# Performance work log

Measured on AMD Instinct MI355X. Metric: run time of the kernel, lower is better.

Reference implementation:

```python
import jax, jax.numpy as jnp
import numpy as np
import math

B, L, D, H = 4, 2048, 1024, 16
HD = D // H


def setup_inputs() -> dict:
    key = jax.random.key(0)
    k1, k2, k3 = jax.random.split(key, 3)
    x = jax.random.normal(k1, (B, L, D), dtype=jnp.float32)
    # Linear weights stored as [in, out] so y = x @ W (equivalent to torch x @ W.T)
    Wqkv = jax.random.normal(k2, (D, 3 * D), dtype=jnp.float32) * (1.0 / math.sqrt(D))
    Wproj = jax.random.normal(k3, (D, D), dtype=jnp.float32) * (1.0 / math.sqrt(D))
    attn_mask = jnp.tril(jnp.ones((L, L), dtype=bool))  # True = attend (causal)
    key_padding_mask = jnp.zeros((B, L), dtype=bool)     # True = padded (none here)
    return {"x": x, "Wqkv": Wqkv, "Wproj": Wproj,
            "attn_mask": attn_mask, "key_padding_mask": key_padding_mask}


def reference(x, Wqkv, Wproj, attn_mask, key_padding_mask):
    Bx, Lx, Dx = x.shape
    qkv = x @ Wqkv                              # [B, L, 3D]
    q, k, v = jnp.split(qkv, 3, axis=-1)
    def shape(t):
        return t.reshape(Bx, Lx, H, HD).transpose(0, 2, 1, 3)  # [B, H, L, hd]
    q, k, v = shape(q), shape(k), shape(v)
    att = jnp.einsum('bhqd,bhkd->bhqk', q, k) / math.sqrt(HD)  # [B, H, L, L]
    neg_inf = jnp.float32(-jnp.inf)
    att = jnp.where(attn_mask[None, None, :, :], att, neg_inf)
    att = jnp.where(key_padding_mask[:, None, None, :], neg_inf, att)
    att = jax.nn.softmax(att, axis=-1)
    y = jnp.einsum('bhqk,bhkd->bhqd', att, v)   # [B, H, L, hd]
    y = y.transpose(0, 2, 1, 3).reshape(Bx, Lx, Dx)
    return y @ Wproj
```

## Files before the change

### kernel.cpp

```cpp
#include <hip/hip_runtime.h>
#include <cstdint>
#include <cstddef>


typedef __attribute__((ext_vector_type(8))) __bf16 bf16x8;
typedef __attribute__((ext_vector_type(4))) __bf16 bf16x4;
typedef __attribute__((ext_vector_type(4))) float f32x4;
typedef __attribute__((ext_vector_type(16))) float f32x16;

__device__ __forceinline__ f32x4 mfma_bf16(bf16x8 a, bf16x8 b, f32x4 c) {
  return __builtin_amdgcn_mfma_f32_16x16x32_bf16(a, b, c, 0, 0, 0);
}

__device__ __forceinline__ f32x16 mfma32(bf16x8 a, bf16x8 b, f32x16 c) {
  return __builtin_amdgcn_mfma_f32_32x32x16_bf16(a, b, c, 0, 0, 0);
}

__device__ __forceinline__ unsigned cvtpk(float a, float b) {
  unsigned r;
  asm("v_cvt_pk_bf16_f32 %0, %1, %2" : "=v"(r) : "v"(a), "v"(b));
  return r;
}

__device__ __forceinline__ void async_copy16(const void* gsrc, void* ldsdst) {
  __builtin_amdgcn_global_load_lds(
      (const __attribute__((address_space(1))) void*)gsrc,
      (__attribute__((address_space(3))) void*)ldsdst, 16, 0, 0);
}

__global__ __launch_bounds__(256) void prep(
    const float* __restrict__ x, __bf16* __restrict__ xb,
    const float* __restrict__ Wqkv, __bf16* __restrict__ WqkvT,
    const float* __restrict__ Wproj, __bf16* __restrict__ WprojT) {
  const int bid = blockIdx.x;
  if (bid < 8192) {
    const size_t i = ((size_t)bid * 256 + threadIdx.x) * 4;
    const float4 v = *(const float4*)&x[i];
    bf16x4 o = {(__bf16)v.x, (__bf16)v.y, (__bf16)v.z, (__bf16)v.w};
    *(bf16x4*)&xb[i] = o;
    return;
  }
  __shared__ float tile[32][33];
  const float* in;
  __bf16* out;
  int idx, gx, R, C;
  if (bid < 8192 + 3072) {
    idx = bid - 8192; in = Wqkv; out = WqkvT; R = 1024; C = 3072; gx = 96;
  } else {
    idx = bid - 11264; in = Wproj; out = WprojT; R = 1024; C = 1024; gx = 32;
  }
  const int c0 = (idx % gx) * 32;
  const int r0 = (idx / gx) * 32;
  const int tx = threadIdx.x & 31;
  const int ty = threadIdx.x >> 5;
#pragma unroll
  for (int i = 0; i < 32; i += 8)
    tile[ty + i][tx] = in[(size_t)(r0 + ty + i) * C + c0 + tx];
  __syncthreads();
#pragma unroll
  for (int i = 0; i < 32; i += 8)
    out[(size_t)(c0 + ty + i) * R + r0 + tx] = (__bf16)tile[tx][ty + i];
}

#define GEMM128x128_CORE(Aptr, Bptr)                                         \
  const int srow32 = tid >> 3;                                    \
  const int schunk = ((tid & 7) ^ (srow32 & 7)) << 3;                        \
  const __bf16* aBase = &(Aptr)[(size_t)(m0 + srow32) * 1024 + schunk];      \
  const __bf16* bBase = &(Bptr)[(size_t)(n0 + srow32) * 1024 + schunk];      \
  auto stgTile = [&](int kt, int b2) {                                       \
    __bf16* dst = smem + b2 * 16384 + wave * 512;                            \
    _Pragma("unroll") for (int u = 0; u < 4; ++u)                            \
        async_copy16(aBase + (size_t)u * 32768 + kt * 64, dst + u * 2048);   \
    _Pragma("unroll") for (int u = 0; u < 4; ++u)                            \
        async_copy16(bBase + (size_t)u * 32768 + kt * 64,                    \
                     dst + 8192 + u * 2048);                                 \
  };                                                                         \
  const f32x4 zero = {0.f, 0.f, 0.f, 0.f};                                   \
  f32x4 acc[4][4];                                                           \
  _Pragma("unroll") for (int i = 0; i < 4; ++i)                              \
      _Pragma("unroll") for (int j = 0; j < 4; ++j) acc[i][j] = zero;        \
  stgTile(0, 0);                                                             \
  asm volatile("s_waitcnt vmcnt(0)" ::: "memory");                           \
  __builtin_amdgcn_s_barrier();                                              \
  for (int t = 0; t < 16; ++t) {                                             \
    const __bf16* As = smem + (t & 1) * 16384;                               \
    const __bf16* Bs = As + 8192;                                            \
    bf16x8 af[4][2], bfr[4][2];                                              \
    _Pragma("unroll") for (int mt = 0; mt < 4; ++mt)                         \
        _Pragma("unroll") for (int kk = 0; kk < 2; ++kk) af[mt][kk] =        \
            *(const bf16x8*)&As[(wr * 64 + mt * 16 + n16) * 64 +             \
                                (((kk * 4 + quad) ^ (n16 & 7)) << 3)];       \
    _Pragma("unroll") for (int nt = 0; nt < 4; ++nt)                         \
        _Pragma("unroll") for (int kk = 0; kk < 2; ++kk) bfr[nt][kk] =       \
            *(const bf16x8*)&Bs[(wc * 64 + nt * 16 + n16) * 64 +             \
                                (((kk * 4 + quad) ^ (n16 & 7)) << 3)];       \
    if (t < 15) stgTile(t + 1, (t + 1) & 1);                                 \
    __builtin_amdgcn_s_barrier();                                            \
    asm volatile("s_waitcnt lgkmcnt(0)" ::: "memory");                       \
    __builtin_amdgcn_sched_barrier(0);                                       \
    __builtin_amdgcn_s_setprio(1);                                           \
    _Pragma("unroll") for (int mt = 0; mt < 4; ++mt)                         \
        _Pragma("unroll") for (int nt = 0; nt < 4; ++nt)                     \
            _Pragma("unroll") for (int kk = 0; kk < 2; ++kk)                 \
                acc[mt][nt] = mfma_bf16(af[mt][kk], bfr[nt][kk],             \
                                        acc[mt][nt]);                        \
    __builtin_amdgcn_s_setprio(0);                                           \
    asm volatile("s_waitcnt vmcnt(0)" ::: "memory");                         \
    __builtin_amdgcn_s_barrier();                                            \
  }

__global__ __launch_bounds__(256, 2) void gemm_qkv(
    const __bf16* __restrict__ A, const __bf16* __restrict__ BT,
    __bf16* __restrict__ Q, __bf16* __restrict__ Kh, __bf16* __restrict__ VT) {
  extern __shared__ __bf16 smem[];
  const int wg = (blockIdx.x & 7) * 192 + (blockIdx.x >> 3);
  const int bm = wg / 24;
  const int bn = wg % 24;
  const int m0 = bm << 7;
  const int n0 = bn << 7;
  const int tid = threadIdx.x;
  const int wave = tid >> 6;
  const int lane = tid & 63;
  const int n16 = lane & 15;
  const int quad = lane >> 4;
  const int wr = wave >> 1;
  const int wc = wave & 1;

  GEMM128x128_CORE(A, BT)

  __bf16* tw = smem + wave * 2048;
  const int b = m0 >> 11;
  const int l0w = (m0 & 2047) + wr * 64;
  const int n = n0 + wc * 64;

  if (n < 2048) {
    const float QSCALE = 0.125f * 1.44269504089f;
    const bool isQ = (n < 1024);
    const int h = (n & 1023) >> 6;
    __bf16* dst = isQ ? Q : Kh;
    const size_t base = ((size_t)(b * 16 + h) * 2048) * 64;
#pragma unroll
    for (int pass = 0; pass < 2; ++pass) {
#pragma unroll
      for (int mt = 2 * pass; mt < 2 * pass + 2; ++mt) {
#pragma unroll
        for (int nt = 0; nt < 4; ++nt)
#pragma unroll
          for (int r = 0; r < 4; ++r) {
            const int hd = nt * 16 + n16;
            const int mm = (mt & 1) * 16 + quad * 4 + r;
            const float v = isQ ? acc[mt][nt][r] * QSCALE : acc[mt][nt][r];
            tw[mm * 64 + (((hd >> 3) ^ (mm & 7)) << 3) + (hd & 7)] =
                (__bf16)v;
          }
      }
#pragma unroll
      for (int i = 0; i < 4; ++i) {
        const int c = lane + 64 * i;
        const int row = c >> 3;
        const int hd0 = (c & 7) << 3;
        const int phys = (c & 7) ^ (row & 7);
        const bf16x8 v = *(const bf16x8*)&tw[row * 64 + phys * 8];
        *(bf16x8*)&dst[base + (size_t)(l0w + pass * 32 + row) * 64 + hd0] = v;
      }
    }
  } else {
    const int h = (n - 2048) >> 6;
    const size_t bhead = (size_t)(b * 16 + h);
#pragma unroll
    for (int pass = 0; pass < 2; ++pass) {
#pragma unroll
      for (int nt = 2 * pass; nt < 2 * pass + 2; ++nt) {
#pragma unroll
        for (int mt = 0; mt < 4; ++mt)
#pragma unroll
          for (int r = 0; r < 4; ++r) {
            const int hdp = (nt & 1) * 16 + n16;
            const int mm = mt * 16 + quad * 4 + r;
            const int phys = (mm >> 3) ^ (hdp & 7);
            tw[hdp * 64 + phys * 8 + (mm & 7)] = (__bf16)acc[mt][nt][r];
          }
      }
#pragma unroll
      for (int i = 0; i < 4; ++i) {
        const int c = lane + 64 * i;
        const int row = c >> 3;
        const int phys = (c & 7) ^ (row & 7);
        const bf16x8 v = *(const bf16x8*)&tw[row * 64 + phys * 8];
        *(bf16x8*)&VT[(bhead * 64 + pass * 32 + row) * 2048 + l0w +
                      (c & 7) * 8] = v;
      }
    }
  }
}

__global__ __launch_bounds__(256, 2) void gemm_bt_f32out(
    const __bf16* __restrict__ A, const __bf16* __restrict__ BT,
    float* __restrict__ C) {
  extern __shared__ __bf16 smem[];
  const int wg = (blockIdx.x & 7) * 64 + (blockIdx.x >> 3);
  const int bm = wg >> 3;
  const int bn = wg & 7;
  const int m0 = bm << 7;
  const int n0 = bn << 7;
  const int tid = threadIdx.x;
  const int wave = tid >> 6;
  const int lane = tid & 63;
  const int n16 = lane & 15;
  const int quad = lane >> 4;
  const int wr = wave >> 1;
  const int wc = wave & 1;

  GEMM128x128_CORE(A, BT)

#pragma unroll
  for (int mt = 0; mt < 4; ++mt) {
#pragma unroll
    for (int r = 0; r < 4; ++r) {
      const int m = m0 + wr * 64 + mt * 16 + quad * 4 + r;
#pragma unroll
      for (int nt = 0; nt < 4; ++nt) {
        const int nn = n0 + wc * 64 + nt * 16 + n16;
        C[(size_t)m * 1024 + nn] = acc[mt][nt][r];
      }
    }
  }
}

__global__ __launch_bounds__(256, 2) void flash_attn(
    const __bf16* __restrict__ Q, const __bf16* __restrict__ Kh,
    const __bf16* __restrict__ VT, __bf16* __restrict__ Y) {
  __shared__ __bf16 Ks[2][2][64 * 64];
  __shared__ __bf16 Vs[2][2][64 * 64];
  const int bh = blockIdx.x;
  const int p = blockIdx.y;
  const int tid = threadIdx.x;
  const int wave = tid >> 6;
  const int lane = tid & 63;
  const int lrow = lane & 31;
  const int hi = lane >> 5;
  const int lswz = lane & 7;
  const __bf16* Qb = Q + (size_t)bh * 2048 * 64;
  const __bf16* Kb = Kh + (size_t)bh * 2048 * 64;
  const __bf16* Vb = VT + (size_t)bh * 64 * 2048;
  const int b = bh >> 4;
  const int h = bh & 15;
  const f32x16 zero16 = {0.f, 0.f, 0.f, 0.f, 0.f, 0.f, 0.f, 0.f,
                         0.f, 0.f, 0.f, 0.f, 0.f, 0.f, 0.f, 0.f};

  const int srow = tid >> 3;
  const int sswz = ((tid & 7) ^ (srow & 7)) << 3;
  const int ldst = wave * 512;

  auto stageKV = [&](int cn, int nb) {
#pragma unroll
    for (int hf = 0; hf < 2; ++hf)
#pragma unroll
      for (int rb = 0; rb < 2; ++rb)
        async_copy16(&Kb[(size_t)(cn + hf * 64 + rb * 32 + srow) * 64 + sswz],
                     &Ks[nb][hf][rb * 2048 + ldst]);
#pragma unroll
    for (int hf = 0; hf < 2; ++hf)
#pragma unroll
      for (int rb = 0; rb < 2; ++rb)
        async_copy16(&Vb[(size_t)(rb * 32 + srow) * 2048 + cn + hf * 64 + sswz],
                     &Vs[nb][hf][rb * 2048 + ldst]);
  };

#pragma unroll
  for (int tt = 0; tt < 2; ++tt) {
    const int t = tt ? 15 - p : p;
    const int q0w = t * 128 + wave * 32;
    const int myq = q0w + lrow;

    bf16x8 qf[4];
#pragma unroll
    for (int i = 0; i < 4; ++i)
      qf[i] = *(const bf16x8*)&Qb[(size_t)myq * 64 + i * 16 + hi * 8];

    f32x16 o0 = zero16, o1 = zero16;
    float lsum = 0.f;
    const int nk = t + 1;

    __syncthreads();
    stageKV(0, 0);

    for (int kt = 0; kt < nk; ++kt) {
      const int buf = kt & 1;
      __syncthreads();
      if (kt + 1 < nk) stageKV((kt + 1) << 7, buf ^ 1);

#pragma unroll
      for (int s = 0; s < 2; ++s) {
        const int c0s = (kt << 7) + (s << 6);
        if (c0s > q0w + 31) continue;
        const __bf16* ks = Ks[buf][s];
        const __bf16* vs = Vs[buf][s];

        f32x16 sc[2];
#pragma unroll
        for (int ch = 0; ch < 2; ++ch) {
          sc[ch] = zero16;
#pragma unroll
          for (int i = 0; i < 4; ++i) {
            const bf16x8 kf = *(const bf16x8*)&ks[(ch * 32 + lrow) * 64 +
                                                  (((2 * i + hi) ^ lswz)
                                                   << 3)];
            sc[ch] = mfma32(kf, qf[i], sc[ch]);
          }
        }
        if (c0s + 63 > q0w) {
#pragma unroll
          for (int ch = 0; ch < 2; ++ch)
#pragma unroll
            for (int r = 0; r < 16; ++r) {
              const int k = c0s + ch * 32 + (r & 3) + 8 * (r >> 2) + 4 * hi;
              float e = __builtin_amdgcn_exp2f(sc[ch][r]);
              e = (k <= myq) ? e : 0.f;
              sc[ch][r] = e;
              lsum += e;
            }
        } else {
#pragma unroll
          for (int ch = 0; ch < 2; ++ch)
#pragma unroll
            for (int r = 0; r < 16; ++r) {
              const float e = __builtin_amdgcn_exp2f(sc[ch][r]);
              sc[ch][r] = e;
              lsum += e;
            }
        }
#pragma unroll
        for (int ch = 0; ch < 2; ++ch) {
#pragma unroll
          for (int kc = 0; kc < 2; ++kc) {
            unsigned c01 = cvtpk(sc[ch][kc * 8 + 0], sc[ch][kc * 8 + 1]);
            unsigned c23 = cvtpk(sc[ch][kc * 8 + 2], sc[ch][kc * 8 + 3]);
            unsigned c45 = cvtpk(sc[ch][kc * 8 + 4], sc[ch][kc * 8 + 5]);
            unsigned c67 = cvtpk(sc[ch][kc * 8 + 6], sc[ch][kc * 8 + 7]);
            asm("v_permlane32_swap_b32 %0, %1" : "+v"(c01), "+v"(c45));
            asm("v_permlane32_swap_b32 %0, %1" : "+v"(c23), "+v"(c67));
            union {
              unsigned u[4];
              bf16x8 v;
            } pu;
            pu.u[0] = c01;
            pu.u[1] = c23;
            pu.u[2] = c45;
            pu.u[3] = c67;
            const int kch = ch * 4 + kc * 2 + hi;
            {
              const bf16x8 vf0 = *(const bf16x8*)&vs[(0 * 32 + lrow) * 64 +
                                                     ((kch ^ lswz) << 3)];
              o0 = mfma32(pu.v, vf0, o0);
              const bf16x8 vf1 = *(const bf16x8*)&vs[(1 * 32 + lrow) * 64 +
                                                     ((kch ^ lswz) << 3)];
              o1 = mfma32(pu.v, vf1, o1);
            }
          }
        }
      }
    }

    lsum += __shfl_xor(lsum, 32);
    const float inv = 1.0f / lsum;
    float invr[16];
#pragma unroll
    for (int r = 0; r < 16; ++r)
      invr[r] = __shfl(inv, (r & 3) + 8 * (r >> 2) + 4 * hi);
#pragma unroll
    for (int r = 0; r < 16; ++r) {
      const int row = q0w + (r & 3) + 8 * (r >> 2) + 4 * hi;
      const size_t yb = (size_t)(b * 2048 + row) * 1024 + h * 64;
      Y[yb + lrow] = (__bf16)(o0[r] * invr[r]);
      Y[yb + 32 + lrow] = (__bf16)(o1[r] * invr[r]);
    }
  }
}

extern "C" void kernel_launch(void* const* d_in, const int* in_sizes, int n_in,
                              void* d_out, int out_size, void* d_ws,
                              size_t ws_size, hipStream_t stream) {
  const float* x = (const float*)d_in[0];
  const float* Wqkv = (const float*)d_in[1];
  const float* Wproj = (const float*)d_in[2];
  float* out = (float*)d_out;

  char* ws = (char*)d_ws;
  __bf16* xb = (__bf16*)ws;     ws += (size_t)8192 * 1024 * 2;
  __bf16* WqkvT = (__bf16*)ws;  ws += (size_t)3072 * 1024 * 2;
  __bf16* WprojT = (__bf16*)ws; ws += (size_t)1024 * 1024 * 2;
  __bf16* Qs = (__bf16*)ws;     ws += (size_t)64 * 2048 * 64 * 2;
  __bf16* Ks = (__bf16*)ws;     ws += (size_t)64 * 2048 * 64 * 2;
  __bf16* VTs = (__bf16*)ws;    ws += (size_t)64 * 64 * 2048 * 2;
  __bf16* attn = xb;

  static bool attrSet = false;
  if (!attrSet) {
    hipFuncSetAttribute((const void*)gemm_qkv,
                        hipFuncAttributeMaxDynamicSharedMemorySize, 65536);
    hipFuncSetAttribute((const void*)gemm_bt_f32out,
                        hipFuncAttributeMaxDynamicSharedMemorySize, 65536);
    attrSet = true;
  }

  prep<<<12288, 256, 0, stream>>>(x, xb, Wqkv, WqkvT, Wproj, WprojT);
  gemm_qkv<<<1536, 256, 65536, stream>>>(xb, WqkvT, Qs, Ks, VTs);
  flash_attn<<<dim3(64, 8), 256, 0, stream>>>(Qs, Ks, VTs, attn);
  gemm_bt_f32out<<<512, 256, 65536, stream>>>(attn, WprojT, out);
}
```

Before: 232.1 us.

## Pipeline flash attention over 64-key steps with a 4-slot ring buffer

Replaces the double-buffered 128-key staging with a 4-slot ring of 64-key K/V tiles, prefetching two steps ahead. Synchronisation changes from __syncthreads to explicit s_waitcnt vmcnt plus raw s_barrier, so only the tile needed next has to have landed. The aim is to overlap global loads with MFMA compute more finely and to cut waiting at barriers. In exchange there are twice as many barriers, and correctness depends on the vmcnt counts matching the number of outstanding async copies.

```diff
diff --git a/kernel.cpp b/kernel.cpp
--- a/kernel.cpp
+++ b/kernel.cpp
@@ -230,8 +230,8 @@
 __global__ __launch_bounds__(256, 2) void flash_attn(
     const __bf16* __restrict__ Q, const __bf16* __restrict__ Kh,
     const __bf16* __restrict__ VT, __bf16* __restrict__ Y) {
-  __shared__ __bf16 Ks[2][2][64 * 64];
-  __shared__ __bf16 Vs[2][2][64 * 64];
+  __shared__ __bf16 Ks[4][64 * 64];
+  __shared__ __bf16 Vs[4][64 * 64];
   const int bh = blockIdx.x;
   const int p = blockIdx.y;
   const int tid = threadIdx.x;
@@ -250,21 +250,18 @@
 
   const int srow = tid >> 3;
   const int sswz = ((tid & 7) ^ (srow & 7)) << 3;
-  const int ldst = wave * 512;
-
-  auto stageKV = [&](int cn, int nb) {
-#pragma unroll
-    for (int hf = 0; hf < 2; ++hf)
-#pragma unroll
-      for (int rb = 0; rb < 2; ++rb)
-        async_copy16(&Kb[(size_t)(cn + hf * 64 + rb * 32 + srow) * 64 + sswz],
-                     &Ks[nb][hf][rb * 2048 + ldst]);
-#pragma unroll
-    for (int hf = 0; hf < 2; ++hf)
-#pragma unroll
-      for (int rb = 0; rb < 2; ++rb)
-        async_copy16(&Vb[(size_t)(rb * 32 + srow) * 2048 + cn + hf * 64 + sswz],
-                     &Vs[nb][hf][rb * 2048 + ldst]);
+  const size_t kg0 = (size_t)srow * 64 + sswz;
+  const size_t kg1 = (size_t)(srow + 32) * 64 + sswz;
+  const size_t vg0 = (size_t)srow * 2048 + sswz;
+  const size_t vg1 = (size_t)(srow + 32) * 2048 + sswz;
+  const int ldst0 = wave * 512;
+  const int ldst1 = 2048 + wave * 512;
+
+  auto stage = [&](int cn, int b4) {
+    async_copy16(&Kb[kg0 + (size_t)cn * 64], &Ks[b4][ldst0]);
+    async_copy16(&Kb[kg1 + (size_t)cn * 64], &Ks[b4][ldst1]);
+    async_copy16(&Vb[vg0 + cn], &Vs[b4][ldst0]);
+    async_copy16(&Vb[vg1 + cn], &Vs[b4][ldst1]);
   };
 
 #pragma unroll
@@ -280,22 +277,22 @@
 
     f32x16 o0 = zero16, o1 = zero16;
     float lsum = 0.f;
-    const int nk = t + 1;
-
-    __syncthreads();
-    stageKV(0, 0);
-
-    for (int kt = 0; kt < nk; ++kt) {
-      const int buf = kt & 1;
-      __syncthreads();
-      if (kt + 1 < nk) stageKV((kt + 1) << 7, buf ^ 1);
-
-#pragma unroll
-      for (int s = 0; s < 2; ++s) {
-        const int c0s = (kt << 7) + (s << 6);
-        if (c0s > q0w + 31) continue;
-        const __bf16* ks = Ks[buf][s];
-        const __bf16* vs = Vs[buf][s];
+    const int nsteps = 2 * (t + 1);
+
+    __builtin_amdgcn_s_barrier();
+    stage(0, 0);
+    stage(64, 1);
+    asm volatile("s_waitcnt vmcnt(4)" ::: "memory");
+    __builtin_amdgcn_s_barrier();
+
+    for (int kt = 0; kt < nsteps; ++kt) {
+      const int c0 = kt << 6;
+      const bool more = (kt + 2 < nsteps);
+      if (more) stage((kt + 2) << 6, (kt + 2) & 3);
+
+      if (c0 <= q0w + 31) {
+        const __bf16* ks = Ks[kt & 3];
+        const __bf16* vs = Vs[kt & 3];
 
         f32x16 sc[2];
 #pragma unroll
@@ -309,12 +306,12 @@
             sc[ch] = mfma32(kf, qf[i], sc[ch]);
           }
         }
-        if (c0s + 63 > q0w) {
+        if (c0 + 63 > q0w) {
 #pragma unroll
           for (int ch = 0; ch < 2; ++ch)
 #pragma unroll
             for (int r = 0; r < 16; ++r) {
-              const int k = c0s + ch * 32 + (r & 3) + 8 * (r >> 2) + 4 * hi;
+              const int k = c0 + ch * 32 + (r & 3) + 8 * (r >> 2) + 4 * hi;
               float e = __builtin_amdgcn_exp2f(sc[ch][r]);
               e = (k <= myq) ? e : 0.f;
               sc[ch][r] = e;
@@ -360,6 +357,14 @@
           }
         }
       }
+
+      if (kt + 1 < nsteps) {
+        if (more)
+          asm volatile("s_waitcnt vmcnt(4)" ::: "memory");
+        else
+          asm volatile("s_waitcnt vmcnt(0)" ::: "memory");
+        __builtin_amdgcn_s_barrier();
+      }
     }
 
     lsum += __shfl_xor(lsum, 32);
```

After: 233.2 us. No clear change (+0.5%).
